# Kernel optimization log

Hardware: AMD Instinct MI355X
Metric: run time of the kernel (lower is better)

## Reference

```python
import jax, jax.numpy as jnp
import numpy as np

B, D, C, K = 1024, 64, 100000, 5  # batch, feature dim, n_classes, positives per sample


def setup_inputs() -> dict:
    key = jax.random.key(0)
    k1, k2, k3 = jax.random.split(key, 3)
    x = jax.random.normal(k1, (B, D), dtype=jnp.float32)
    W = jax.random.normal(k2, (D, C), dtype=jnp.float32) * 0.02
    b = jnp.zeros((C,), dtype=jnp.float32)
    # K distinct positive class ids per sample (setdiff1d assume_unique requires distinct)
    base = jax.random.randint(k3, (B, 1), 0, C)
    labels = (base + jnp.arange(K, dtype=jnp.int64)[None, :]) % C
    return {"x": x, "labels": labels, "W": W, "b": b}


def reference(x, labels, W, b):
    # classifier: logits [B, C]
    logits = x @ W + b
    # Original loop: for each positive p of a sample, CE over [p] + negatives
    # (negatives = all classes except ALL positives of that sample), label 0:
    #   loss_p = -(l_p - log(exp(l_p) + sum_{c in negatives} exp(l_c)))
    # Vectorized via total expsum minus the positives' contribution.
    m = jnp.max(logits, axis=1, keepdims=True)                    # [B, 1]
    e = jnp.exp(logits - m)                                       # [B, C]
    total = jnp.sum(e, axis=1, keepdims=True)                     # [B, 1]
    pos_logits = jnp.take_along_axis(logits, labels, axis=1)      # [B, K]
    pos_e = jnp.exp(pos_logits - m)                               # [B, K]
    neg_sum = total - jnp.sum(pos_e, axis=1, keepdims=True)       # [B, 1]
    denom = pos_e + neg_sum                                       # [B, K]
    losses = -(pos_logits - m - jnp.log(denom))                   # [B, K]
    # sum over all (sample, positive) pairs / total number of positives
    return jnp.sum(losses) / losses.size
```

## Files before the change

kernel.cpp:

```cpp
#include <hip/hip_runtime.h>

constexpr int Bn = 1024;
constexpr int Dn = 64;
constexpr int Cn = 100000;
constexpr int Kn = 5;
constexpr float LOG2E = 1.44269504088896f;
constexpr float LN2   = 0.69314718055994531f;

typedef float f32x4  __attribute__((ext_vector_type(4)));
typedef short bf16x8 __attribute__((ext_vector_type(8)));

__device__ __forceinline__ unsigned short f32_to_bf16(float f) {
  union { float f; unsigned int u; } v; v.f = f;
  unsigned int r = v.u + 0x7FFFu + ((v.u >> 16) & 1u);
  return (unsigned short)(r >> 16);
}
__device__ __forceinline__ float bf16_to_f32(unsigned short u) {
  union { unsigned int i; float f; } v; v.i = ((unsigned int)u) << 16; return v.f;
}

constexpr int SPLITS = 125;
constexpr int CPS    = Cn / SPLITS;
constexpr int NCH    = CPS / 32;
constexpr int SGRPS  = 8;
constexpr int GRID   = SPLITS * SGRPS;
constexpr int TP     = 88;

__global__ __launch_bounds__(256) void fused_gemm_kernel(
    const float* __restrict__ x, const float* __restrict__ W,
    const float* __restrict__ bias, float* __restrict__ P,
    float* __restrict__ out)
{
  __shared__ unsigned short wt[2][32][TP];

  const int b   = blockIdx.x;
  const int tid = threadIdx.x;
  if (b == 0 && tid == 0) *out = 0.f;

  const int xcd = b & 7, bs = b >> 3;
  const int wgid  = xcd * 125 + bs;
  const int split = wgid >> 3, sgrp = wgid & 7;

  const int lane = tid & 63, wid = tid >> 6;
  const int lr = lane & 15, lg = lane >> 4;
  const int sbase = sgrp * 128 + wid * 32;
  const int cb0   = split * CPS;

  bf16x8 a[2][2];
#pragma unroll
  for (int t = 0; t < 2; ++t) {
    const float* xp = x + (size_t)(sbase + t * 16 + lr) * 64 + lg * 8;
    const float4 v0 = *reinterpret_cast<const float4*>(xp);
    const float4 v1 = *reinterpret_cast<const float4*>(xp + 4);
    const float4 v2 = *reinterpret_cast<const float4*>(xp + 32);
    const float4 v3 = *reinterpret_cast<const float4*>(xp + 36);
    bf16x8 a0, a1;
    a0[0] = (short)f32_to_bf16(v0.x * LOG2E);
    a0[1] = (short)f32_to_bf16(v0.y * LOG2E);
    a0[2] = (short)f32_to_bf16(v0.z * LOG2E);
    a0[3] = (short)f32_to_bf16(v0.w * LOG2E);
    a0[4] = (short)f32_to_bf16(v1.x * LOG2E);
    a0[5] = (short)f32_to_bf16(v1.y * LOG2E);
    a0[6] = (short)f32_to_bf16(v1.z * LOG2E);
    a0[7] = (short)f32_to_bf16(v1.w * LOG2E);
    a1[0] = (short)f32_to_bf16(v2.x * LOG2E);
    a1[1] = (short)f32_to_bf16(v2.y * LOG2E);
    a1[2] = (short)f32_to_bf16(v2.z * LOG2E);
    a1[3] = (short)f32_to_bf16(v2.w * LOG2E);
    a1[4] = (short)f32_to_bf16(v3.x * LOG2E);
    a1[5] = (short)f32_to_bf16(v3.y * LOG2E);
    a1[6] = (short)f32_to_bf16(v3.z * LOG2E);
    a1[7] = (short)f32_to_bf16(v3.w * LOG2E);
    a[t][0] = a0;
    a[t][1] = a1;
  }

  const int sd = tid >> 3;
  const int sc = (tid & 7) * 4;
  const float* wrow0 = W + (size_t)sd * Cn;
  const float* wrow1 = W + (size_t)(sd + 32) * Cn;

  {
    const float4 v0 = *reinterpret_cast<const float4*>(wrow0 + cb0 + sc);
    const float4 v1 = *reinterpret_cast<const float4*>(wrow1 + cb0 + sc);
#pragma unroll
    for (int j = 0; j < 4; ++j) {
      wt[0][sc + j][sd]      = f32_to_bf16(v0[j]);
      wt[0][sc + j][sd + 32] = f32_to_bf16(v1[j]);
    }
  }
  __syncthreads();

  float esum[2][4];
#pragma unroll
  for (int t = 0; t < 2; ++t)
#pragma unroll
    for (int j = 0; j < 4; ++j) esum[t][j] = 0.f;

#pragma unroll 1
  for (int ch = 0; ch < NCH; ++ch) {
    float4 n0, n1;
    const bool more = (ch + 1 < NCH);
    if (more) {
      const int cbn = cb0 + (ch + 1) * 32;
      n0 = *reinterpret_cast<const float4*>(wrow0 + cbn + sc);
      n1 = *reinterpret_cast<const float4*>(wrow1 + cbn + sc);
    }

    const int cur = ch & 1;
    const int cb  = cb0 + ch * 32;
    const float bb0 = bias[cb + lr] * LOG2E;
    const float bb1 = bias[cb + 16 + lr] * LOG2E;
    const bf16x8 b00 = *reinterpret_cast<const bf16x8*>(&wt[cur][lr][lg * 8]);
    const bf16x8 b01 = *reinterpret_cast<const bf16x8*>(&wt[cur][lr][32 + lg * 8]);
    const bf16x8 b10 = *reinterpret_cast<const bf16x8*>(&wt[cur][16 + lr][lg * 8]);
    const bf16x8 b11 = *reinterpret_cast<const bf16x8*>(&wt[cur][16 + lr][32 + lg * 8]);

#pragma unroll
    for (int t = 0; t < 2; ++t) {
      f32x4 acc0 = {bb0, bb0, bb0, bb0};
      f32x4 acc1 = {bb1, bb1, bb1, bb1};
      acc0 = __builtin_amdgcn_mfma_f32_16x16x32_bf16(a[t][0], b00, acc0, 0, 0, 0);
      acc1 = __builtin_amdgcn_mfma_f32_16x16x32_bf16(a[t][0], b10, acc1, 0, 0, 0);
      acc0 = __builtin_amdgcn_mfma_f32_16x16x32_bf16(a[t][1], b01, acc0, 0, 0, 0);
      acc1 = __builtin_amdgcn_mfma_f32_16x16x32_bf16(a[t][1], b11, acc1, 0, 0, 0);
#pragma unroll
      for (int j = 0; j < 4; ++j) {
        const float e0 = __builtin_amdgcn_exp2f(acc0[j]);
        const float e1 = __builtin_amdgcn_exp2f(acc1[j]);
        esum[t][j] += e0 + e1;
      }
    }

    if (more) {
      const int nb = (ch + 1) & 1;
#pragma unroll
      for (int j = 0; j < 4; ++j) {
        wt[nb][sc + j][sd]      = f32_to_bf16(n0[j]);
        wt[nb][sc + j][sd + 32] = f32_to_bf16(n1[j]);
      }
    }
    __syncthreads();
  }

  float red[2][4];
#pragma unroll
  for (int t = 0; t < 2; ++t)
#pragma unroll
    for (int j = 0; j < 4; ++j) {
      float v = esum[t][j];
      v += __shfl_xor(v, 1, 64);
      v += __shfl_xor(v, 2, 64);
      v += __shfl_xor(v, 4, 64);
      v += __shfl_xor(v, 8, 64);
      red[t][j] = v;
    }
  if (lr == 0) {
#pragma unroll
    for (int t = 0; t < 2; ++t)
#pragma unroll
      for (int j = 0; j < 4; ++j)
        P[(size_t)(sbase + t * 16 + lg * 4 + j) * SPLITS + split] = red[t][j];
  }
}

__global__ __launch_bounds__(64) void loss3_kernel(
    const float* __restrict__ x, const int* __restrict__ labels,
    const float* __restrict__ W, const float* __restrict__ bias,
    const float* __restrict__ P, float* __restrict__ out)
{
  const int i = blockIdx.x, lane = threadIdx.x;
  float acc = P[(size_t)i * SPLITS + lane];
  if (lane + 64 < SPLITS) acc += P[(size_t)i * SPLITS + lane + 64];
#pragma unroll
  for (int off = 32; off > 0; off >>= 1) acc += __shfl_xor(acc, off, 64);
  const float Si = acc;

  const float xv = bf16_to_f32(f32_to_bf16(x[i * Dn + lane] * LOG2E));
  float l2[Kn];
#pragma unroll
  for (int p = 0; p < Kn; ++p) {
    const int c = labels[i * Kn + p];
    const float wv = bf16_to_f32(f32_to_bf16(W[(size_t)lane * Cn + c]));
    float v = xv * wv;
#pragma unroll
    for (int off = 32; off > 0; off >>= 1) v += __shfl_xor(v, off, 64);
    l2[p] = v + bias[c] * LOG2E;
  }
  if (lane == 0) {
    float Psum = 0.f;
#pragma unroll
    for (int p = 0; p < Kn; ++p) Psum += __builtin_amdgcn_exp2f(l2[p]);
    const float neg = Si - Psum;
    float lsum = 0.f;
#pragma unroll
    for (int p = 0; p < Kn; ++p)
      lsum += __logf(__builtin_amdgcn_exp2f(l2[p]) + neg) - l2[p] * LN2;
    atomicAdd(out, lsum * (1.0f / (float)(Bn * Kn)));
  }
}

constexpr int NB  = 128;
constexpr int NPB = (Cn + NB - 1) / NB;
constexpr int NPBpad = 784;

__global__ __launch_bounds__(256) void cvt_x_kernel(
    const float* __restrict__ x, unsigned short* __restrict__ xb)
{
  const int i = (blockIdx.x * 256 + threadIdx.x) * 4;
  const float4 v = *reinterpret_cast<const float4*>(x + i);
  ushort4 o;
  o.x = f32_to_bf16(v.x); o.y = f32_to_bf16(v.y);
  o.z = f32_to_bf16(v.z); o.w = f32_to_bf16(v.w);
  *reinterpret_cast<ushort4*>(xb + i) = o;
}

__global__ __launch_bounds__(256) void expsum_mfma_kernel(
    const unsigned short* __restrict__ xb, const float* __restrict__ W,
    const float* __restrict__ bias, float* __restrict__ P,
    float* __restrict__ S, int use_partials)
{
  __shared__ float S_lds[4][Bn];
  const int tid  = threadIdx.x;
  const int lane = tid & 63, wid = tid >> 6;
  const int lg = lane >> 4, lr = lane & 15;
  const int cbase = blockIdx.x * NB + wid * 32;

  for (int i = tid; i < 4 * Bn; i += 256) (&S_lds[0][0])[i] = 0.f;

  bf16x8 bfrag[2][2];
  float  bval[2];
#pragma unroll
  for (int t = 0; t < 2; ++t) {
    const int c  = cbase + t * 16 + lr;
    const bool ok = (c < Cn);
    bval[t] = ok ? bias[c] * LOG2E : -1e38f;
#pragma unroll
    for (int h = 0; h < 2; ++h) {
      bf16x8 bf;
#pragma unroll
      for (int j = 0; j < 8; ++j) {
        const int d = h * 32 + lg * 8 + j;
        const float w = ok ? W[(size_t)d * Cn + c] : 0.f;
        bf[j] = (short)f32_to_bf16(w);
      }
      bfrag[t][h] = bf;
    }
  }
  __syncthreads();

#pragma unroll 1
  for (int ch = 0; ch < Bn / 16; ++ch) {
    const int s = ch * 16 + lr;
    const bf16x8 a0 = *reinterpret_cast<const bf16x8*>(xb + (size_t)s * Dn + lg * 8);
    const bf16x8 a1 = *reinterpret_cast<const bf16x8*>(xb + (size_t)s * Dn + 32 + lg * 8);
    f32x4 acc0 = {0.f, 0.f, 0.f, 0.f};
    f32x4 acc1 = {0.f, 0.f, 0.f, 0.f};
    acc0 = __builtin_amdgcn_mfma_f32_16x16x32_bf16(a0, bfrag[0][0], acc0, 0, 0, 0);
    acc1 = __builtin_amdgcn_mfma_f32_16x16x32_bf16(a0, bfrag[1][0], acc1, 0, 0, 0);
    acc0 = __builtin_amdgcn_mfma_f32_16x16x32_bf16(a1, bfrag[0][1], acc0, 0, 0, 0);
    acc1 = __builtin_amdgcn_mfma_f32_16x16x32_bf16(a1, bfrag[1][1], acc1, 0, 0, 0);

    float v[4];
#pragma unroll
    for (int j = 0; j < 4; ++j) {
      const float e0 = __builtin_amdgcn_exp2f(fmaf(acc0[j], LOG2E, bval[0]));
      const float e1 = __builtin_amdgcn_exp2f(fmaf(acc1[j], LOG2E, bval[1]));
      v[j] = e0 + e1;
    }
#pragma unroll
    for (int j = 0; j < 4; ++j) {
      v[j] += __shfl_xor(v[j], 1, 64);
      v[j] += __shfl_xor(v[j], 2, 64);
      v[j] += __shfl_xor(v[j], 4, 64);
      v[j] += __shfl_xor(v[j], 8, 64);
    }
    if (lr == 0) {
#pragma unroll
      for (int j = 0; j < 4; ++j)
        S_lds[wid][ch * 16 + lg * 4 + j] += v[j];
    }
  }
  __syncthreads();

  if (use_partials) {
    for (int s2 = tid; s2 < Bn; s2 += 256) {
      const float v = S_lds[0][s2] + S_lds[1][s2] + S_lds[2][s2] + S_lds[3][s2];
      P[(size_t)s2 * NPBpad + blockIdx.x] = v;
    }
  } else {
    for (int s2 = tid; s2 < Bn; s2 += 256) {
      const float v = S_lds[0][s2] + S_lds[1][s2] + S_lds[2][s2] + S_lds[3][s2];
      atomicAdd(&S[s2], v);
    }
  }
}

__global__ __launch_bounds__(64) void loss_kernel(
    const float* __restrict__ x, const int* __restrict__ labels,
    const float* __restrict__ W, const float* __restrict__ bias,
    const float* __restrict__ P, const float* __restrict__ S,
    float* __restrict__ out, int use_partials)
{
  const int i    = blockIdx.x;
  const int lane = threadIdx.x;

  float Si;
  if (use_partials) {
    float acc = 0.f;
    for (int j = lane; j < NPB; j += 64) acc += P[(size_t)i * NPBpad + j];
#pragma unroll
    for (int off = 32; off > 0; off >>= 1) acc += __shfl_xor(acc, off, 64);
    Si = acc;
  } else {
    Si = S[i];
  }

  const float xv = x[i * Dn + lane];
  float l[Kn];
#pragma unroll
  for (int p = 0; p < Kn; ++p) {
    const int c = labels[i * Kn + p];
    float v = xv * W[(size_t)lane * Cn + c];
#pragma unroll
    for (int off = 32; off > 0; off >>= 1) v += __shfl_xor(v, off, 64);
    l[p] = v + bias[c];
  }

  if (lane == 0) {
    float Psum = 0.f;
#pragma unroll
    for (int p = 0; p < Kn; ++p) Psum += __expf(l[p]);
    const float neg = Si - Psum;
    float lsum = 0.f;
#pragma unroll
    for (int p = 0; p < Kn; ++p)
      lsum += __logf(__expf(l[p]) + neg) - l[p];
    atomicAdd(out, lsum * (1.0f / (float)(Bn * Kn)));
  }
}

extern "C" void kernel_launch(void* const* d_in, const int* in_sizes, int n_in,
                              void* d_out, int out_size, void* d_ws, size_t ws_size,
                              hipStream_t stream) {
  const float* x      = (const float*)d_in[0];
  const int*   labels = (const int*)d_in[1];
  const float* W      = (const float*)d_in[2];
  const float* bias   = (const float*)d_in[3];
  float*       out    = (float*)d_out;
  char*        ws     = (char*)d_ws;

  const size_t need_new = (size_t)SPLITS * Bn * 4;

  if (ws_size >= need_new) {
    float* P = (float*)ws;
    fused_gemm_kernel<<<GRID, 256, 0, stream>>>(x, W, bias, P, out);
    loss3_kernel<<<Bn, 64, 0, stream>>>(x, labels, W, bias, P, out);
    return;
  }

  hipMemsetAsync(out, 0, sizeof(float), stream);
  float*          Sg = (float*)ws;
  unsigned short* xb = (unsigned short*)(ws + 4096);
  float*          Pp = (float*)(ws + 4096 + (size_t)Bn * Dn * 2);
  const size_t need_old = 4096 + (size_t)Bn * Dn * 2 + (size_t)Bn * NPBpad * 4;
  const int use_partials = (ws_size >= need_old) ? 1 : 0;
  if (!use_partials) hipMemsetAsync(Sg, 0, Bn * sizeof(float), stream);

  cvt_x_kernel<<<(Bn * Dn) / (256 * 4), 256, 0, stream>>>(x, xb);
  expsum_mfma_kernel<<<NPB, 256, 0, stream>>>(xb, W, bias, Pp, Sg, use_partials);
  loss_kernel<<<Bn, 64, 0, stream>>>(x, labels, W, bias, Pp, Sg, out, use_partials);
}
```

Measured before the change: 52.51 us.

## Use 512-thread blocks covering 256 samples and scalar-load W tiles with vector LDS stores

Doubles the block size so each workgroup covers 256 samples instead of 128. This halves the grid and the number of times each W chunk is loaded and converted to bf16. The W staging changes from float4 row loads with scattered 2-byte LDS stores to four strided scalar global loads per thread followed by one 8-byte LDS store. The XCD-aware workgroup remap is rebuilt for the 500-block grid. The cost is fewer blocks for latency hiding, and the global loads, while still coalesced across threads, are scalar rather than vector.

```diff
diff --git a/kernel.cpp b/kernel.cpp
--- a/kernel.cpp
+++ b/kernel.cpp
@@ -22,11 +22,11 @@
 constexpr int SPLITS = 125;
 constexpr int CPS    = Cn / SPLITS;
 constexpr int NCH    = CPS / 32;
-constexpr int SGRPS  = 8;
+constexpr int SGRPS  = 4;
 constexpr int GRID   = SPLITS * SGRPS;
 constexpr int TP     = 88;
 
-__global__ __launch_bounds__(256) void fused_gemm_kernel(
+__global__ __launch_bounds__(512) void fused_gemm_kernel(
     const float* __restrict__ x, const float* __restrict__ W,
     const float* __restrict__ bias, float* __restrict__ P,
     float* __restrict__ out)
@@ -38,12 +38,12 @@
   if (b == 0 && tid == 0) *out = 0.f;
 
   const int xcd = b & 7, bs = b >> 3;
-  const int wgid  = xcd * 125 + bs;
-  const int split = wgid >> 3, sgrp = wgid & 7;
+  const int wgid = (xcd < 4 ? xcd * 63 : 252 + (xcd - 4) * 62) + bs;
+  const int split = wgid >> 2, sgrp = wgid & 3;
 
   const int lane = tid & 63, wid = tid >> 6;
   const int lr = lane & 15, lg = lane >> 4;
-  const int sbase = sgrp * 128 + wid * 32;
+  const int sbase = sgrp * 256 + wid * 32;
   const int cb0   = split * CPS;
 
   bf16x8 a[2][2];
@@ -75,19 +75,18 @@
     a[t][1] = a1;
   }
 
-  const int sd = tid >> 3;
-  const int sc = (tid & 7) * 4;
-  const float* wrow0 = W + (size_t)sd * Cn;
-  const float* wrow1 = W + (size_t)(sd + 32) * Cn;
+  const int sclass = tid >> 4;
+  const int sdq    = tid & 15;
+  const float* wbase = W + (size_t)(sdq * 4) * Cn;
 
   {
-    const float4 v0 = *reinterpret_cast<const float4*>(wrow0 + cb0 + sc);
-    const float4 v1 = *reinterpret_cast<const float4*>(wrow1 + cb0 + sc);
-#pragma unroll
-    for (int j = 0; j < 4; ++j) {
-      wt[0][sc + j][sd]      = f32_to_bf16(v0[j]);
-      wt[0][sc + j][sd + 32] = f32_to_bf16(v1[j]);
-    }
+    float v[4];
+#pragma unroll
+    for (int j = 0; j < 4; ++j) v[j] = wbase[(size_t)j * Cn + (cb0 + sclass)];
+    ushort4 o;
+    o.x = f32_to_bf16(v[0]); o.y = f32_to_bf16(v[1]);
+    o.z = f32_to_bf16(v[2]); o.w = f32_to_bf16(v[3]);
+    *reinterpret_cast<ushort4*>(&wt[0][sclass][sdq * 4]) = o;
   }
   __syncthreads();
 
@@ -99,12 +98,12 @@
 
 #pragma unroll 1
   for (int ch = 0; ch < NCH; ++ch) {
-    float4 n0, n1;
+    float n[4];
     const bool more = (ch + 1 < NCH);
     if (more) {
-      const int cbn = cb0 + (ch + 1) * 32;
-      n0 = *reinterpret_cast<const float4*>(wrow0 + cbn + sc);
-      n1 = *reinterpret_cast<const float4*>(wrow1 + cbn + sc);
+      const int cbn = cb0 + (ch + 1) * 32 + sclass;
+#pragma unroll
+      for (int j = 0; j < 4; ++j) n[j] = wbase[(size_t)j * Cn + cbn];
     }
 
     const int cur = ch & 1;
@@ -134,11 +133,10 @@
 
     if (more) {
       const int nb = (ch + 1) & 1;
-#pragma unroll
-      for (int j = 0; j < 4; ++j) {
-        wt[nb][sc + j][sd]      = f32_to_bf16(n0[j]);
-        wt[nb][sc + j][sd + 32] = f32_to_bf16(n1[j]);
-      }
+      ushort4 o;
+      o.x = f32_to_bf16(n[0]); o.y = f32_to_bf16(n[1]);
+      o.z = f32_to_bf16(n[2]); o.w = f32_to_bf16(n[3]);
+      *reinterpret_cast<ushort4*>(&wt[nb][sclass][sdq * 4]) = o;
     }
     __syncthreads();
   }
@@ -354,7 +352,7 @@
 
   if (ws_size >= need_new) {
     float* P = (float*)ws;
-    fused_gemm_kernel<<<GRID, 256, 0, stream>>>(x, W, bias, P, out);
+    fused_gemm_kernel<<<GRID, 512, 0, stream>>>(x, W, bias, P, out);
     loss3_kernel<<<Bn, 64, 0, stream>>>(x, labels, W, bias, P, out);
     return;
   }
```

Result: slower. 76.56 us (+45.8%).

## Pre-convert W to swizzled bf16 and stream tiles via direct global-to-LDS loads

Applied to the files above, without the earlier changes.

A new prep kernel converts W to bf16 once per call, stores it transposed per class with an XOR swizzle, and writes it to a workspace buffer. The GEMM/expsum kernel then reads that buffer with global_load_lds directly into a 4-deep LDS ring, two chunks per barrier, and no longer converts data in registers. The aim is to cut the per-chunk conversion and transpose work and the number of barriers. The cost is an extra kernel launch, an extra write and read of a 12.8MB bf16 copy of W, and a larger workspace requirement.

```diff
diff --git a/kernel.cpp b/kernel.cpp
--- a/kernel.cpp
+++ b/kernel.cpp
@@ -19,23 +19,60 @@
   union { unsigned int i; float f; } v; v.i = ((unsigned int)u) << 16; return v.f;
 }
 
+__device__ __forceinline__ void gl2lds16(const void* g, void* l) {
+  __builtin_amdgcn_global_load_lds(
+      (const __attribute__((address_space(1))) void*)g,
+      (__attribute__((address_space(3))) void*)l, 16, 0, 0);
+}
+
 constexpr int SPLITS = 125;
 constexpr int CPS    = Cn / SPLITS;
 constexpr int NCH    = CPS / 32;
 constexpr int SGRPS  = 8;
 constexpr int GRID   = SPLITS * SGRPS;
-constexpr int TP     = 88;
-
-__global__ __launch_bounds__(256) void fused_gemm_kernel(
-    const float* __restrict__ x, const float* __restrict__ W,
-    const float* __restrict__ bias, float* __restrict__ P,
+constexpr int NBLK_W = (Cn + 63) / 64;
+
+__global__ __launch_bounds__(256) void prep_kernel(
+    const float* __restrict__ W, unsigned short* __restrict__ Wt,
     float* __restrict__ out)
 {
-  __shared__ unsigned short wt[2][32][TP];
+  __shared__ unsigned short tile[64][71];
+  const int tid = threadIdx.x;
+  const int b   = blockIdx.x;
+  if (b == 0 && tid == 0) *out = 0.f;
+
+  const int c0   = b * 64;
+  const int cIdx = tid & 63, dIdx = tid >> 6;
+#pragma unroll
+  for (int k = 0; k < 16; ++k) {
+    const int d = dIdx * 16 + k;
+    const int c = c0 + cIdx;
+    const float v = (c < Cn) ? W[(size_t)d * Cn + c] : 0.f;
+    tile[d][cIdx] = f32_to_bf16(v);
+  }
+  __syncthreads();
+  const int cl = tid >> 2, dq = tid & 3;
+  if (c0 + cl < Cn) {
+    bf16x8 o0, o1;
+#pragma unroll
+    for (int k = 0; k < 8; ++k) o0[k] = (short)tile[dq * 16 + k][cl];
+#pragma unroll
+    for (int k = 0; k < 8; ++k) o1[k] = (short)tile[dq * 16 + 8 + k][cl];
+    const int swz = cl & 7;
+    unsigned short* rowp = Wt + (size_t)(c0 + cl) * 64;
+    *reinterpret_cast<bf16x8*>(rowp + ((2 * dq)     ^ swz) * 8) = o0;
+    *reinterpret_cast<bf16x8*>(rowp + ((2 * dq + 1) ^ swz) * 8) = o1;
+  }
+}
+
+__global__ __launch_bounds__(256) void gemm_gl_kernel(
+    const float* __restrict__ x, const unsigned short* __restrict__ Wt,
+    const float* __restrict__ bias, float* __restrict__ P)
+{
+  __shared__ unsigned short wl[4][32 * 64];
 
   const int b   = blockIdx.x;
   const int tid = threadIdx.x;
-  if (b == 0 && tid == 0) *out = 0.f;
 
   const int xcd = b & 7, bs = b >> 3;
   const int wgid  = xcd * 125 + bs;
@@ -75,20 +112,13 @@
     a[t][1] = a1;
   }
 
-  const int sd = tid >> 3;
-  const int sc = (tid & 7) * 4;
-  const float* wrow0 = W + (size_t)sd * Cn;
-  const float* wrow1 = W + (size_t)(sd + 32) * Cn;
-
-  {
-    const float4 v0 = *reinterpret_cast<const float4*>(wrow0 + cb0 + sc);
-    const float4 v1 = *reinterpret_cast<const float4*>(wrow1 + cb0 + sc);
-#pragma unroll
-    for (int j = 0; j < 4; ++j) {
-      wt[0][sc + j][sd]      = f32_to_bf16(v0[j]);
-      wt[0][sc + j][sd + 32] = f32_to_bf16(v1[j]);
-    }
-  }
+  const unsigned short* gsrc0 = Wt + (size_t)cb0 * 64 + tid * 8;
+  const int ro0 = lr * 64, ro1 = (16 + lr) * 64;
+  const int s0 = ((lg ^ (lr & 7)) << 3);
+  const int s1 = (((4 + lg) ^ (lr & 7)) << 3);
+
+  gl2lds16(gsrc0,            &wl[0][wid * 512]);
+  gl2lds16(gsrc0 + 32 * 64,  &wl[1][wid * 512]);
   __syncthreads();
 
   float esum[2][4];
@@ -98,46 +128,39 @@
     for (int j = 0; j < 4; ++j) esum[t][j] = 0.f;
 
 #pragma unroll 1
-  for (int ch = 0; ch < NCH; ++ch) {
-    float4 n0, n1;
-    const bool more = (ch + 1 < NCH);
-    if (more) {
-      const int cbn = cb0 + (ch + 1) * 32;
-      n0 = *reinterpret_cast<const float4*>(wrow0 + cbn + sc);
-      n1 = *reinterpret_cast<const float4*>(wrow1 + cbn + sc);
-    }
-
-    const int cur = ch & 1;
-    const int cb  = cb0 + ch * 32;
-    const float bb0 = bias[cb + lr] * LOG2E;
-    const float bb1 = bias[cb + 16 + lr] * LOG2E;
-    const bf16x8 b00 = *reinterpret_cast<const bf16x8*>(&wt[cur][lr][lg * 8]);
-    const bf16x8 b01 = *reinterpret_cast<const bf16x8*>(&wt[cur][lr][32 + lg * 8]);
-    const bf16x8 b10 = *reinterpret_cast<const bf16x8*>(&wt[cur][16 + lr][lg * 8]);
-    const bf16x8 b11 = *reinterpret_cast<const bf16x8*>(&wt[cur][16 + lr][32 + lg * 8]);
-
-#pragma unroll
-    for (int t = 0; t < 2; ++t) {
-      f32x4 acc0 = {bb0, bb0, bb0, bb0};
-      f32x4 acc1 = {bb1, bb1, bb1, bb1};
-      acc0 = __builtin_amdgcn_mfma_f32_16x16x32_bf16(a[t][0], b00, acc0, 0, 0, 0);
-      acc1 = __builtin_amdgcn_mfma_f32_16x16x32_bf16(a[t][0], b10, acc1, 0, 0, 0);
-      acc0 = __builtin_amdgcn_mfma_f32_16x16x32_bf16(a[t][1], b01, acc0, 0, 0, 0);
-      acc1 = __builtin_amdgcn_mfma_f32_16x16x32_bf16(a[t][1], b11, acc1, 0, 0, 0);
-#pragma unroll
-      for (int j = 0; j < 4; ++j) {
-        const float e0 = __builtin_amdgcn_exp2f(acc0[j]);
-        const float e1 = __builtin_amdgcn_exp2f(acc1[j]);
-        esum[t][j] += e0 + e1;
-      }
-    }
-
-    if (more) {
-      const int nb = (ch + 1) & 1;
-#pragma unroll
-      for (int j = 0; j < 4; ++j) {
-        wt[nb][sc + j][sd]      = f32_to_bf16(n0[j]);
-        wt[nb][sc + j][sd + 32] = f32_to_bf16(n1[j]);
+  for (int ch = 0; ch < NCH; ch += 2) {
+    if (ch + 2 < NCH)
+      gl2lds16(gsrc0 + (size_t)(ch + 2) * 32 * 64, &wl[(ch + 2) & 3][wid * 512]);
+    if (ch + 3 < NCH)
+      gl2lds16(gsrc0 + (size_t)(ch + 3) * 32 * 64, &wl[(ch + 3) & 3][wid * 512]);
+
+#pragma unroll
+    for (int e = 0; e < 2; ++e) {
+      const int c = ch + e;
+      if (c < NCH) {
+        const unsigned short* wb = wl[c & 3];
+        const int cb = cb0 + c * 32;
+        const float bb0 = bias[cb + lr] * LOG2E;
+        const float bb1 = bias[cb + 16 + lr] * LOG2E;
+        const bf16x8 b00 = *reinterpret_cast<const bf16x8*>(&wb[ro0 + s0]);
+        const bf16x8 b01 = *reinterpret_cast<const bf16x8*>(&wb[ro0 + s1]);
+        const bf16x8 b10 = *reinterpret_cast<const bf16x8*>(&wb[ro1 + s0]);
+        const bf16x8 b11 = *reinterpret_cast<const bf16x8*>(&wb[ro1 + s1]);
+#pragma unroll
+        for (int t = 0; t < 2; ++t) {
+          f32x4 acc0 = {bb0, bb0, bb0, bb0};
+          f32x4 acc1 = {bb1, bb1, bb1, bb1};
+          acc0 = __builtin_amdgcn_mfma_f32_16x16x32_bf16(a[t][0], b00, acc0, 0, 0, 0);
+          acc1 = __builtin_amdgcn_mfma_f32_16x16x32_bf16(a[t][0], b10, acc1, 0, 0, 0);
+          acc0 = __builtin_amdgcn_mfma_f32_16x16x32_bf16(a[t][1], b01, acc0, 0, 0, 0);
+          acc1 = __builtin_amdgcn_mfma_f32_16x16x32_bf16(a[t][1], b11, acc1, 0, 0, 0);
+#pragma unroll
+          for (int j = 0; j < 4; ++j) {
+            const float e0 = __builtin_amdgcn_exp2f(acc0[j]);
+            const float e1 = __builtin_amdgcn_exp2f(acc1[j]);
+            esum[t][j] += e0 + e1;
+          }
+        }
       }
     }
     __syncthreads();
@@ -350,11 +373,15 @@
   float*       out    = (float*)d_out;
   char*        ws     = (char*)d_ws;
 
-  const size_t need_new = (size_t)SPLITS * Bn * 4;
+  const size_t off_P  = 0;
+  const size_t off_Wt = (size_t)SPLITS * Bn * 4;
+  const size_t need_new = off_Wt + (size_t)Cn * Dn * 2;
 
   if (ws_size >= need_new) {
-    float* P = (float*)ws;
-    fused_gemm_kernel<<<GRID, 256, 0, stream>>>(x, W, bias, P, out);
+    float*          P  = (float*)(ws + off_P);
+    unsigned short* Wt = (unsigned short*)(ws + off_Wt);
+    prep_kernel<<<NBLK_W, 256, 0, stream>>>(W, Wt, out);
+    gemm_gl_kernel<<<GRID, 256, 0, stream>>>(x, Wt, bias, P);
     loss3_kernel<<<Bn, 64, 0, stream>>>(x, labels, W, bias, P, out);
     return;
   }
```

Result: slower. 58.93 us (+12.2%).
